# Optimization experiments

Hardware: AMD Instinct MI355X
Metric: run time of the kernel (lower is better)

The kernel has to match this reference:

```python
import jax, jax.numpy as jnp
import numpy as np

POOL_SIZE = 7


def _pool_matrix(dim_size: int, pool_size: int) -> np.ndarray:
    # Faithful to torch.linspace(0, dim, pool_size+1, dtype=torch.int):
    # float linspace then truncation toward zero.
    bins = np.linspace(0, dim_size, pool_size + 1).astype(np.int64)
    P = np.zeros((pool_size, dim_size), dtype=np.float32)
    for i in range(pool_size):
        s, e = int(bins[i]), int(bins[i + 1])
        P[i, s:e] = 1.0 / (e - s)
    return P


def setup_inputs() -> dict:
    key = jax.random.key(0)
    x = jax.random.normal(key, (32, 2048, 28, 28), dtype=jnp.float32)
    return {"x": x}


def reference(x) -> jnp.ndarray:
    B, C, H, W = x.shape
    Ph = jnp.asarray(_pool_matrix(H, POOL_SIZE))  # [P, H], row i averages bin i
    Pw = jnp.asarray(_pool_matrix(W, POOL_SIZE))  # [P, W]
    # out[b, i, j, c] = mean of x[b, c, h_bin_i, w_bin_j]
    out = jnp.einsum('bchw,ih,jw->bijc', x, Ph, Pw)  # [B, P, P, C]
    return out.reshape(B, POOL_SIZE * POOL_SIZE, C)  # [B, 49, C], matches torch stack order (i-major)
```

## Files before the change

kernel.cpp:

```cpp
#include <hip/hip_runtime.h>


#define CH 2048
#define OUT_PER_B (49 * CH)

__global__ __launch_bounds__(256) void upp_pool_kernel(const float* __restrict__ x,
                                                       float* __restrict__ out) {
    __shared__ float scratch[4][200];
    __shared__ float res[49][65];

    const int wave = threadIdx.x >> 6;
    const int lane = threadIdx.x & 63;
    const int b    = blockIdx.x >> 5;
    const int c0   = (blockIdx.x & 31) * 64;

    float* myLds = scratch[wave];
    const float* imgBase = x + ((size_t)b * CH + c0 + wave * 16) * 784;

    const int bi   = lane / 7;
    const int bj   = lane - bi * 7;
    const int bofs = bi * 28 + bj;

    for (int it = 0; it < 16; ++it) {
        const float4* img = (const float4*)(imgBase + (size_t)it * 784);

        const float4 v0 = img[lane];
        const float4 v1 = img[lane + 64];
        const float4 v2 = img[lane + 128];
        myLds[lane]       = (v0.x + v0.y) + (v0.z + v0.w);
        myLds[lane + 64]  = (v1.x + v1.y) + (v1.z + v1.w);
        myLds[lane + 128] = (v2.x + v2.y) + (v2.z + v2.w);
        if (lane < 4) {
            const float4 v3 = img[192 + lane];
            myLds[192 + lane] = (v3.x + v3.y) + (v3.z + v3.w);
        }

        __syncthreads();

        if (lane < 49) {
            const float s = (myLds[bofs] + myLds[bofs + 7]) +
                            (myLds[bofs + 14] + myLds[bofs + 21]);
            res[lane][wave * 16 + it] = s * (1.0f / 16.0f);
        }

        __syncthreads();
    }

    float* outBase = out + (size_t)b * OUT_PER_B + c0;
    for (int p = wave; p < 49; p += 4) {
        outBase[(size_t)p * CH + lane] = res[p][lane];
    }
}

extern "C" void kernel_launch(void* const* d_in, const int* in_sizes, int n_in,
                              void* d_out, int out_size, void* d_ws, size_t ws_size,
                              hipStream_t stream) {
    const float* x = (const float*)d_in[0];
    float* out = (float*)d_out;

    upp_pool_kernel<<<1024, 256, 0, stream>>>(x, out);
}
```

Baseline: 281.7 us.

## Prefetch next channel image into registers and drop per-iteration block barriers

Each wave now loads the next 28x28 channel slice into registers while it reduces the current one, using a double-buffered per-wave LDS scratch. The two __syncthreads per iteration are replaced by a single barrier before the final store. The loop is fully unrolled. This is meant to keep more global loads in flight and cut barrier stalls in a latency-bound loop, at the cost of extra registers and reliance on wave-synchronous LDS ordering within a wave.

```diff
diff --git a/kernel.cpp b/kernel.cpp
--- a/kernel.cpp
+++ b/kernel.cpp
@@ -4,9 +4,13 @@
 #define CH 2048
 #define OUT_PER_B (49 * CH)
 
+__device__ __forceinline__ float hsum4(float4 v) {
+    return (v.x + v.y) + (v.z + v.w);
+}
+
 __global__ __launch_bounds__(256) void upp_pool_kernel(const float* __restrict__ x,
                                                        float* __restrict__ out) {
-    __shared__ float scratch[4][200];
+    __shared__ float scratch[4][2][200];
     __shared__ float res[49][65];
 
     const int wave = threadIdx.x >> 6;
@@ -14,39 +18,52 @@
     const int b    = blockIdx.x >> 5;
     const int c0   = (blockIdx.x & 31) * 64;
 
-    float* myLds = scratch[wave];
     const float* imgBase = x + ((size_t)b * CH + c0 + wave * 16) * 784;
 
     const int bi   = lane / 7;
     const int bj   = lane - bi * 7;
     const int bofs = bi * 28 + bj;
 
+    float4 a0, a1, a2, a3;
+    {
+        const float4* img = (const float4*)imgBase;
+        a0 = img[lane];
+        a1 = img[lane + 64];
+        a2 = img[lane + 128];
+        a3 = (lane < 4) ? img[192 + lane] : make_float4(0.f, 0.f, 0.f, 0.f);
+    }
+
+#pragma unroll
     for (int it = 0; it < 16; ++it) {
-        const float4* img = (const float4*)(imgBase + (size_t)it * 784);
-
-        const float4 v0 = img[lane];
-        const float4 v1 = img[lane + 64];
-        const float4 v2 = img[lane + 128];
-        myLds[lane]       = (v0.x + v0.y) + (v0.z + v0.w);
-        myLds[lane + 64]  = (v1.x + v1.y) + (v1.z + v1.w);
-        myLds[lane + 128] = (v2.x + v2.y) + (v2.z + v2.w);
-        if (lane < 4) {
-            const float4 v3 = img[192 + lane];
-            myLds[192 + lane] = (v3.x + v3.y) + (v3.z + v3.w);
+        float4 b0, b1, b2, b3;
+        b0 = b1 = b2 = b3 = make_float4(0.f, 0.f, 0.f, 0.f);
+        if (it < 15) {
+            const float4* img = (const float4*)(imgBase + (size_t)(it + 1) * 784);
+            b0 = img[lane];
+            b1 = img[lane + 64];
+            b2 = img[lane + 128];
+            if (lane < 4) b3 = img[192 + lane];
         }
 
-        __syncthreads();
+        float* L = scratch[wave][it & 1];
+        L[lane]       = hsum4(a0);
+        L[lane + 64]  = hsum4(a1);
+        L[lane + 128] = hsum4(a2);
+        if (lane < 4) L[192 + lane] = hsum4(a3);
 
         if (lane < 49) {
-            const float s = (myLds[bofs] + myLds[bofs + 7]) +
-                            (myLds[bofs + 14] + myLds[bofs + 21]);
+            const float s = (L[bofs] + L[bofs + 7]) +
+                            (L[bofs + 14] + L[bofs + 21]);
             res[lane][wave * 16 + it] = s * (1.0f / 16.0f);
         }
 
-        __syncthreads();
+        a0 = b0; a1 = b1; a2 = b2; a3 = b3;
     }
 
+    __syncthreads();
+
     float* outBase = out + (size_t)b * OUT_PER_B + c0;
+#pragma unroll
     for (int p = wave; p < 49; p += 4) {
         outBase[(size_t)p * CH + lane] = res[p][lane];
     }
```

Result: no change. 282.5 us (+0.3%).
